# Performance work log

Hardware: AMD Instinct MI355X
Metric: run time of the kernel (lower is better)

Reference implementation:

```python
import jax, jax.numpy as jnp
import numpy as np

N_NODES = 100000
N_EDGES = 1600000
NFEAT = 128
NHID = 64
DEC_HID = 128


def setup_inputs() -> dict:
    key = jax.random.key(0)
    ks = jax.random.split(key, 12)
    s = lambda fan_in: 1.0 / np.sqrt(fan_in)
    x = jax.random.normal(ks[0], (N_NODES, NFEAT), dtype=jnp.float32)
    edge_index = jax.random.randint(ks[1], (2, N_EDGES), 0, N_NODES, dtype=jnp.int32)
    W1 = jax.random.normal(ks[2], (NFEAT, NHID), dtype=jnp.float32) * s(NFEAT)
    W2 = jax.random.normal(ks[3], (NHID, NHID), dtype=jnp.float32) * s(NHID)
    Wx1 = jax.random.normal(ks[4], (NHID, DEC_HID), dtype=jnp.float32) * s(NHID)
    bx1 = jnp.zeros((DEC_HID,), dtype=jnp.float32)
    Wx2 = jax.random.normal(ks[5], (DEC_HID, NFEAT), dtype=jnp.float32) * s(DEC_HID)
    bx2 = jnp.zeros((NFEAT,), dtype=jnp.float32)
    Wh1 = jax.random.normal(ks[6], (NHID, DEC_HID), dtype=jnp.float32) * s(NHID)
    bh1 = jnp.zeros((DEC_HID,), dtype=jnp.float32)
    Wh2 = jax.random.normal(ks[7], (DEC_HID, NFEAT), dtype=jnp.float32) * s(DEC_HID)
    bh2 = jnp.zeros((NFEAT,), dtype=jnp.float32)
    return {"x": x, "edge_index": edge_index, "W1": W1, "W2": W2,
            "Wx1": Wx1, "bx1": bx1, "Wx2": Wx2, "bx2": bx2,
            "Wh1": Wh1, "bh1": bh1, "Wh2": Wh2, "bh2": bh2}


def _segsum(vals, idx, n):
    return jax.ops.segment_sum(vals, idx, num_segments=n)


def reference(x, edge_index, W1, W2, Wx1, bx1, Wx2, bx2, Wh1, bh1, Wh2, bh2):
    N = x.shape[0]
    src, dst = edge_index[0], edge_index[1]
    ones_e = jnp.ones((src.shape[0],), dtype=x.dtype)
    in_cnt = _segsum(ones_e, dst, N)                       # [N] in-degree
    deg = in_cnt + 1.0                                     # +1 for self-loop
    dinv = jax.lax.rsqrt(deg)
    enorm = dinv[src] * dinv[dst]                          # [E] symmetric norm

    def gcn_layer(h, W):
        m = h @ W                                          # transform first [N,H]
        agg = _segsum(m[src] * enorm[:, None], dst, N)     # gather+scatter
        return agg + m / deg[:, None]                      # self-loop term

    h = jax.nn.relu(gcn_layer(x, W1))
    h = gcn_layer(h, W2)                                   # [N, nhid]

    # dec_x MLP (dropout=0 in eval)
    x_hat = jax.nn.relu(h @ Wx1 + bx1) @ Wx2 + bx2         # [N, nfeat]

    # neighbor_mean: scatter_mean of h[src] onto dst
    cnt = jnp.maximum(in_cnt, 1.0)
    h_bar = _segsum(h[src], dst, N) / cnt[:, None]         # [N, nhid]
    m_hat = jax.nn.relu(h_bar @ Wh1 + bh1) @ Wh2 + bh2     # [N, nfeat]

    return (h, x_hat, m_hat)
```

## Files before the change

### kernel.cpp

```cpp
#include <hip/hip_runtime.h>


#define BUCK_SHIFT 7
#define BUCK_W 128
#define MAXB 1024
#define EMIT_CHUNK 8192


__global__ __launch_bounds__(256) void bucket_count(const int* __restrict__ dst,
                                                    int* __restrict__ bucketCnt,
                                                    int E, int NBUCK) {
    __shared__ int h[MAXB];
    for (int i = threadIdx.x; i < NBUCK; i += 256) h[i] = 0;
    __syncthreads();
    for (long long e = (long long)blockIdx.x * blockDim.x + threadIdx.x; e < E;
         e += (long long)gridDim.x * blockDim.x)
        atomicAdd(&h[dst[e] >> BUCK_SHIFT], 1);
    __syncthreads();
    for (int i = threadIdx.x; i < NBUCK; i += 256)
        if (h[i]) atomicAdd(&bucketCnt[i], h[i]);
}

__global__ __launch_bounds__(1024) void bucket_scan(const int* __restrict__ cnt,
                                                    int* __restrict__ off,
                                                    int* __restrict__ cur,
                                                    int NBUCK, int E) {
    __shared__ int s[1024];
    const int t = threadIdx.x;
    int v = (t < NBUCK) ? cnt[t] : 0;
    s[t] = v;
    __syncthreads();
    for (int o = 1; o < 1024; o <<= 1) {
        int u = (t >= o) ? s[t - o] : 0;
        __syncthreads();
        s[t] += u;
        __syncthreads();
    }
    if (t < NBUCK) { off[t] = s[t] - v; cur[t] = s[t] - v; }
    if (t == 0) off[NBUCK] = E;
}

__global__ __launch_bounds__(256) void bucket_emit(const int* __restrict__ src,
                                                   const int* __restrict__ dst,
                                                   int* __restrict__ bucketCursor,
                                                   uint2* __restrict__ staging,
                                                   int E, int NBUCK) {
    __shared__ int h[MAXB];
    const int t = threadIdx.x;
    const long long base = (long long)blockIdx.x * EMIT_CHUNK;
    for (int i = t; i < NBUCK; i += 256) h[i] = 0;
    __syncthreads();
#pragma unroll
    for (int i = 0; i < EMIT_CHUNK / 256; ++i) {
        long long e = base + t + i * 256;
        if (e < E) atomicAdd(&h[dst[e] >> BUCK_SHIFT], 1);
    }
    __syncthreads();
    for (int i = t; i < NBUCK; i += 256) {
        int c = h[i];
        h[i] = c ? atomicAdd(&bucketCursor[i], c) : 0;
    }
    __syncthreads();
#pragma unroll
    for (int i = 0; i < EMIT_CHUNK / 256; ++i) {
        long long e = base + t + i * 256;
        if (e < E) {
            int d = dst[e];
            int pos = atomicAdd(&h[d >> BUCK_SHIFT], 1);
            staging[pos] = make_uint2((unsigned)src[e], (unsigned)d);
        }
    }
}

__global__ __launch_bounds__(256) void bucket_sort(const uint2* __restrict__ staging,
                                                   const int* __restrict__ bucketOff,
                                                   int* __restrict__ rowStart,
                                                   int* __restrict__ adj,
                                                   int N, int NBUCK, int E) {
    __shared__ int h[BUCK_W];
    __shared__ int cur[BUCK_W];
    const int b = blockIdx.x;
    const int t = threadIdx.x;
    const int lo = b << BUCK_SHIFT;
    const int off = bucketOff[b];
    const int M = bucketOff[b + 1] - off;
    if (t < BUCK_W) h[t] = 0;
    __syncthreads();
    for (int i = t; i < M; i += 256)
        atomicAdd(&h[(int)staging[off + i].y - lo], 1);
    __syncthreads();
    if (t < BUCK_W) cur[t] = h[t];
    __syncthreads();
    for (int o = 1; o < BUCK_W; o <<= 1) {
        int u = 0;
        if (t < BUCK_W && t >= o) u = cur[t - o];
        __syncthreads();
        if (t < BUCK_W) cur[t] += u;
        __syncthreads();
    }
    if (t < BUCK_W) {
        int ex = off + cur[t] - h[t];
        int d = lo + t;
        if (d < N) rowStart[d] = ex;
        cur[t] = ex;
    }
    if (b == 0 && t == 0) rowStart[N] = E;
    __syncthreads();
    for (int i = t; i < M; i += 256) {
        uint2 p = staging[off + i];
        int pos = atomicAdd(&cur[(int)p.y - lo], 1);
        adj[pos] = (int)p.x;
    }
}

__global__ void dinv_kernel(const int* __restrict__ rowStart, float* __restrict__ dinv, int N) {
    int i = blockIdx.x * blockDim.x + threadIdx.x;
    if (i < N) {
        int deg = rowStart[i + 1] - rowStart[i];
        dinv[i] = rsqrtf((float)deg + 1.0f);
    }
}

template <int K>
__global__ __launch_bounds__(256) void gemm64(const float* __restrict__ A,
                                              const float* __restrict__ W,
                                              float* __restrict__ out, int N) {
    const int tx = threadIdx.x;
    const int c4 = (tx & 15) << 2;
    const int rg = (tx >> 4) << 2;
    const int row0 = blockIdx.x * 64;
    __shared__ float As[64][K + 1];
    constexpr int C4 = K / 4;
    for (int idx = tx; idx < 64 * C4; idx += 256) {
        int r = idx / C4, c = idx - r * C4;
        int row = row0 + r;
        float4 v = (row < N) ? ((const float4*)A)[(long long)row * C4 + c]
                             : make_float4(0.f, 0.f, 0.f, 0.f);
        As[r][c * 4 + 0] = v.x;
        As[r][c * 4 + 1] = v.y;
        As[r][c * 4 + 2] = v.z;
        As[r][c * 4 + 3] = v.w;
    }
    __syncthreads();
    float acc[4][4];
#pragma unroll
    for (int r = 0; r < 4; ++r)
#pragma unroll
        for (int j = 0; j < 4; ++j) acc[r][j] = 0.f;
#pragma unroll 8
    for (int k = 0; k < K; ++k) {
        float4 w = *(const float4*)&W[k * 64 + c4];
        float a0 = As[rg + 0][k];
        float a1 = As[rg + 1][k];
        float a2 = As[rg + 2][k];
        float a3 = As[rg + 3][k];
        acc[0][0] += a0 * w.x; acc[0][1] += a0 * w.y; acc[0][2] += a0 * w.z; acc[0][3] += a0 * w.w;
        acc[1][0] += a1 * w.x; acc[1][1] += a1 * w.y; acc[1][2] += a1 * w.z; acc[1][3] += a1 * w.w;
        acc[2][0] += a2 * w.x; acc[2][1] += a2 * w.y; acc[2][2] += a2 * w.z; acc[2][3] += a2 * w.w;
        acc[3][0] += a3 * w.x; acc[3][1] += a3 * w.y; acc[3][2] += a3 * w.z; acc[3][3] += a3 * w.w;
    }
#pragma unroll
    for (int r = 0; r < 4; ++r) {
        int row = row0 + rg + r;
        if (row < N)
            *(float4*)&out[(long long)row * 64 + c4] =
                make_float4(acc[r][0], acc[r][1], acc[r][2], acc[r][3]);
    }
}

template <int RELU>
__global__ __launch_bounds__(256) void gather_combine4(const float4* __restrict__ m4,
                                                       const int* __restrict__ rowStart,
                                                       const int* __restrict__ adj,
                                                       const float* __restrict__ dinv,
                                                       float4* __restrict__ out4, int N) {
    int gid = blockIdx.x * 256 + threadIdx.x;
    int d = gid >> 4;
    if (d >= N) return;
    int l = gid & 15;
    int start = rowStart[d], end = rowStart[d + 1];
    float dv = dinv[d];
    float4 ms = m4[(long long)d * 16 + l];
    float4 a0, a1;
    a0.x = ms.x * dv; a0.y = ms.y * dv; a0.z = ms.z * dv; a0.w = ms.w * dv;
    a1.x = 0.f; a1.y = 0.f; a1.z = 0.f; a1.w = 0.f;
    int t = start;
    for (; t + 2 <= end; t += 2) {
        int s0 = adj[t], s1 = adj[t + 1];
        float w0 = dinv[s0], w1 = dinv[s1];
        float4 v0 = m4[(long long)s0 * 16 + l];
        float4 v1 = m4[(long long)s1 * 16 + l];
        a0.x += v0.x * w0; a0.y += v0.y * w0; a0.z += v0.z * w0; a0.w += v0.w * w0;
        a1.x += v1.x * w1; a1.y += v1.y * w1; a1.z += v1.z * w1; a1.w += v1.w * w1;
    }
    if (t < end) {
        int s = adj[t];
        float w = dinv[s];
        float4 v = m4[(long long)s * 16 + l];
        a0.x += v.x * w; a0.y += v.y * w; a0.z += v.z * w; a0.w += v.w * w;
    }
    float4 r;
    r.x = (a0.x + a1.x) * dv; r.y = (a0.y + a1.y) * dv;
    r.z = (a0.z + a1.z) * dv; r.w = (a0.w + a1.w) * dv;
    if (RELU) {
        r.x = fmaxf(r.x, 0.f); r.y = fmaxf(r.y, 0.f);
        r.z = fmaxf(r.z, 0.f); r.w = fmaxf(r.w, 0.f);
    }
    out4[(long long)d * 16 + l] = r;
}

__global__ __launch_bounds__(256) void gather_mean4(const float4* __restrict__ h4,
                                                    const int* __restrict__ rowStart,
                                                    const int* __restrict__ adj,
                                                    float4* __restrict__ out4, int N) {
    int gid = blockIdx.x * 256 + threadIdx.x;
    int d = gid >> 4;
    if (d >= N) return;
    int l = gid & 15;
    int start = rowStart[d], end = rowStart[d + 1];
    int deg = end - start;
    float4 a0, a1;
    a0.x = 0.f; a0.y = 0.f; a0.z = 0.f; a0.w = 0.f;
    a1 = a0;
    int t = start;
    for (; t + 2 <= end; t += 2) {
        int s0 = adj[t], s1 = adj[t + 1];
        float4 v0 = h4[(long long)s0 * 16 + l];
        float4 v1 = h4[(long long)s1 * 16 + l];
        a0.x += v0.x; a0.y += v0.y; a0.z += v0.z; a0.w += v0.w;
        a1.x += v1.x; a1.y += v1.y; a1.z += v1.z; a1.w += v1.w;
    }
    if (t < end) {
        float4 v = h4[(long long)adj[t] * 16 + l];
        a0.x += v.x; a0.y += v.y; a0.z += v.z; a0.w += v.w;
    }
    float inv = 1.0f / (float)max(deg, 1);
    float4 r;
    r.x = (a0.x + a1.x) * inv; r.y = (a0.y + a1.y) * inv;
    r.z = (a0.z + a1.z) * inv; r.w = (a0.w + a1.w) * inv;
    out4[(long long)d * 16 + l] = r;
}

__global__ __launch_bounds__(256) void mlp2_dual(const float* __restrict__ In0,
                                                 const float* __restrict__ In1,
                                                 const float* __restrict__ Wa0,
                                                 const float* __restrict__ ba0,
                                                 const float* __restrict__ Wb0,
                                                 const float* __restrict__ bb0,
                                                 const float* __restrict__ Wa1,
                                                 const float* __restrict__ ba1,
                                                 const float* __restrict__ Wb1,
                                                 const float* __restrict__ bb1,
                                                 float* __restrict__ out0,
                                                 float* __restrict__ out1, int N) {
    const int which = blockIdx.y;
    const float* In = which ? In1 : In0;
    const float* Wa = which ? Wa1 : Wa0;
    const float* ba = which ? ba1 : ba0;
    const float* Wb = which ? Wb1 : Wb0;
    const float* bb = which ? bb1 : bb0;
    float* out = which ? out1 : out0;

    const int tx = threadIdx.x;
    const int c4 = (tx & 31) << 2;
    const int rg = (tx >> 5) << 3;
    const int row0 = blockIdx.x * 64;
    __shared__ float ins[64][64];
    __shared__ float t[64][128];
    for (int idx = tx; idx < 64 * 16; idx += 256) {
        int r = idx >> 4, c = idx & 15;
        int row = row0 + r;
        float4 v = (row < N) ? ((const float4*)In)[(long long)row * 16 + c]
                             : make_float4(0.f, 0.f, 0.f, 0.f);
        *(float4*)&ins[r][c * 4] = v;
    }
    __syncthreads();
    float acc[8][4];
    float4 b1 = *(const float4*)&ba[c4];
#pragma unroll
    for (int r = 0; r < 8; ++r) {
        acc[r][0] = b1.x; acc[r][1] = b1.y; acc[r][2] = b1.z; acc[r][3] = b1.w;
    }
#pragma unroll 8
    for (int k = 0; k < 64; ++k) {
        float4 w = *(const float4*)&Wa[k * 128 + c4];
#pragma unroll
        for (int r = 0; r < 8; ++r) {
            float a = ins[rg + r][k];
            acc[r][0] += a * w.x; acc[r][1] += a * w.y;
            acc[r][2] += a * w.z; acc[r][3] += a * w.w;
        }
    }
#pragma unroll
    for (int r = 0; r < 8; ++r)
        *(float4*)&t[rg + r][c4] = make_float4(fmaxf(acc[r][0], 0.f), fmaxf(acc[r][1], 0.f),
                                               fmaxf(acc[r][2], 0.f), fmaxf(acc[r][3], 0.f));
    __syncthreads();
    float4 b2 = *(const float4*)&bb[c4];
#pragma unroll
    for (int r = 0; r < 8; ++r) {
        acc[r][0] = b2.x; acc[r][1] = b2.y; acc[r][2] = b2.z; acc[r][3] = b2.w;
    }
#pragma unroll 8
    for (int k = 0; k < 128; ++k) {
        float4 w = *(const float4*)&Wb[k * 128 + c4];
#pragma unroll
        for (int r = 0; r < 8; ++r) {
            float a = t[rg + r][k];
            acc[r][0] += a * w.x; acc[r][1] += a * w.y;
            acc[r][2] += a * w.z; acc[r][3] += a * w.w;
        }
    }
#pragma unroll
    for (int r = 0; r < 8; ++r) {
        int row = row0 + rg + r;
        if (row < N)
            *(float4*)&out[(long long)row * 128 + c4] =
                make_float4(acc[r][0], acc[r][1], acc[r][2], acc[r][3]);
    }
}

extern "C" void kernel_launch(void* const* d_in, const int* in_sizes, int n_in,
                              void* d_out, int out_size, void* d_ws, size_t ws_size,
                              hipStream_t stream) {
    const float* x   = (const float*)d_in[0];
    const int*   ei  = (const int*)  d_in[1];
    const float* W1  = (const float*)d_in[2];
    const float* W2  = (const float*)d_in[3];
    const float* Wx1 = (const float*)d_in[4];
    const float* bx1 = (const float*)d_in[5];
    const float* Wx2 = (const float*)d_in[6];
    const float* bx2 = (const float*)d_in[7];
    const float* Wh1 = (const float*)d_in[8];
    const float* bh1 = (const float*)d_in[9];
    const float* Wh2 = (const float*)d_in[10];
    const float* bh2 = (const float*)d_in[11];

    const int NFEAT = 128, NHID = 64;
    const int N = in_sizes[0] / NFEAT;
    const int E = in_sizes[1] / 2;
    const int NBUCK = (N + BUCK_W - 1) >> BUCK_SHIFT;

    float* out   = (float*)d_out;
    float* h_out = out;
    float* xhat  = out + (long long)N * NHID;
    float* mhat  = xhat + (long long)N * NFEAT;

    char* wsb = (char*)d_ws;
    int*   adj       = (int*)wsb;        wsb += (size_t)E * 4;
    int*   rowStart  = (int*)wsb;        wsb += (size_t)(N + 2) * 4;
    int*   bucketCnt = (int*)wsb;        wsb += (size_t)MAXB * 4;
    int*   bucketOff = (int*)wsb;        wsb += (size_t)(MAXB + 2) * 4;
    int*   bucketCur = (int*)wsb;        wsb += (size_t)MAXB * 4;
    float* dinv      = (float*)wsb;      wsb += (size_t)N * 4;
    float* mbuf      = (float*)wsb;      wsb += (size_t)N * 64 * 4;
    float* hbuf      = (float*)wsb;
    uint2* staging   = (uint2*)mbuf;

    const int B = 256;
    const int gridN   = (N + B - 1) / B;
    const int gridG   = (N + 63) / 64;
    const int gridGa  = ((N * 16) + B - 1) / B;
    const int gridEm  = (E + EMIT_CHUNK - 1) / EMIT_CHUNK;
    dim3 gridMLP((N + 63) / 64, 2);

    const int* srcp = ei;
    const int* dstp = ei + E;

    hipMemsetAsync(bucketCnt, 0, (size_t)MAXB * 4, stream);
    bucket_count<<<256, 256, 0, stream>>>(dstp, bucketCnt, E, NBUCK);
    bucket_scan<<<1, 1024, 0, stream>>>(bucketCnt, bucketOff, bucketCur, NBUCK, E);
    bucket_emit<<<gridEm, 256, 0, stream>>>(srcp, dstp, bucketCur, staging, E, NBUCK);
    bucket_sort<<<NBUCK, 256, 0, stream>>>(staging, bucketOff, rowStart, adj, N, NBUCK, E);
    dinv_kernel<<<gridN, B, 0, stream>>>(rowStart, dinv, N);

    gemm64<128><<<gridG, B, 0, stream>>>(x, W1, mbuf, N);
    gather_combine4<1><<<gridGa, B, 0, stream>>>((const float4*)mbuf, rowStart, adj, dinv,
                                                 (float4*)hbuf, N);

    gemm64<64><<<gridG, B, 0, stream>>>(hbuf, W2, mbuf, N);
    gather_combine4<0><<<gridGa, B, 0, stream>>>((const float4*)mbuf, rowStart, adj, dinv,
                                                 (float4*)h_out, N);

    gather_mean4<<<gridGa, B, 0, stream>>>((const float4*)h_out, rowStart, adj,
                                           (float4*)mbuf, N);

    mlp2_dual<<<gridMLP, B, 0, stream>>>(h_out, mbuf,
                                         Wx1, bx1, Wx2, bx2,
                                         Wh1, bh1, Wh2, bh2,
                                         xhat, mhat, N);
}
```

Measured before the change: 661.6 us.

## Stage decoder MLP weights in shared memory with chunked reuse buffer

The fused two-layer decoder MLP kernel now copies the first-layer weight matrix and 32-row chunks of the second-layer weights into one shared buffer. It no longer reads them from global memory inside the inner loop. The same buffer is reused for the input tile, the hidden activations and the weight chunks, keeping shared memory at 48 KB. The cost is extra barriers between chunks, and loading weights is serialized with compute.

```diff
diff --git a/kernel.cpp b/kernel.cpp
--- a/kernel.cpp
+++ b/kernel.cpp
@@ -265,16 +265,19 @@
     const int c4 = (tx & 31) << 2;
     const int rg = (tx >> 5) << 3;
     const int row0 = blockIdx.x * 64;
-    __shared__ float ins[64][64];
-    __shared__ float t[64][128];
-    for (int idx = tx; idx < 64 * 16; idx += 256) {
+    __shared__ float buf[12288];
+
+    for (int idx = tx; idx < 1024; idx += 256) {
         int r = idx >> 4, c = idx & 15;
         int row = row0 + r;
         float4 v = (row < N) ? ((const float4*)In)[(long long)row * 16 + c]
                              : make_float4(0.f, 0.f, 0.f, 0.f);
-        *(float4*)&ins[r][c * 4] = v;
-    }
-    __syncthreads();
+        *(float4*)&buf[r * 64 + c * 4] = v;
+    }
+    for (int idx = tx; idx < 2048; idx += 256)
+        *(float4*)&buf[4096 + idx * 4] = ((const float4*)Wa)[idx];
+    __syncthreads();
+
     float acc[8][4];
     float4 b1 = *(const float4*)&ba[c4];
 #pragma unroll
@@ -283,32 +286,47 @@
     }
 #pragma unroll 8
     for (int k = 0; k < 64; ++k) {
-        float4 w = *(const float4*)&Wa[k * 128 + c4];
+        float4 w = *(const float4*)&buf[4096 + k * 128 + c4];
 #pragma unroll
         for (int r = 0; r < 8; ++r) {
-            float a = ins[rg + r][k];
+            float a = buf[(rg + r) * 64 + k];
             acc[r][0] += a * w.x; acc[r][1] += a * w.y;
             acc[r][2] += a * w.z; acc[r][3] += a * w.w;
         }
     }
+    __syncthreads();
+
 #pragma unroll
     for (int r = 0; r < 8; ++r)
-        *(float4*)&t[rg + r][c4] = make_float4(fmaxf(acc[r][0], 0.f), fmaxf(acc[r][1], 0.f),
-                                               fmaxf(acc[r][2], 0.f), fmaxf(acc[r][3], 0.f));
-    __syncthreads();
+        *(float4*)&buf[4096 + (rg + r) * 128 + c4] =
+            make_float4(fmaxf(acc[r][0], 0.f), fmaxf(acc[r][1], 0.f),
+                        fmaxf(acc[r][2], 0.f), fmaxf(acc[r][3], 0.f));
+    for (int idx = tx; idx < 1024; idx += 256)
+        *(float4*)&buf[idx * 4] = ((const float4*)Wb)[idx];
+    __syncthreads();
+
     float4 b2 = *(const float4*)&bb[c4];
 #pragma unroll
     for (int r = 0; r < 8; ++r) {
         acc[r][0] = b2.x; acc[r][1] = b2.y; acc[r][2] = b2.z; acc[r][3] = b2.w;
     }
+    for (int q = 0; q < 4; ++q) {
+        const int k0 = q * 32;
 #pragma unroll 8
-    for (int k = 0; k < 128; ++k) {
-        float4 w = *(const float4*)&Wb[k * 128 + c4];
-#pragma unroll
-        for (int r = 0; r < 8; ++r) {
-            float a = t[rg + r][k];
-            acc[r][0] += a * w.x; acc[r][1] += a * w.y;
-            acc[r][2] += a * w.z; acc[r][3] += a * w.w;
+        for (int k = 0; k < 32; ++k) {
+            float4 w = *(const float4*)&buf[k * 128 + c4];
+#pragma unroll
+            for (int r = 0; r < 8; ++r) {
+                float a = buf[4096 + (rg + r) * 128 + k0 + k];
+                acc[r][0] += a * w.x; acc[r][1] += a * w.y;
+                acc[r][2] += a * w.z; acc[r][3] += a * w.w;
+            }
+        }
+        if (q < 3) {
+            __syncthreads();
+            for (int idx = tx; idx < 1024; idx += 256)
+                *(float4*)&buf[idx * 4] = ((const float4*)Wb)[(q + 1) * 1024 + idx];
+            __syncthreads();
         }
     }
 #pragma unroll
```

Result: slower. 686.7 us (+3.8%).
